# Kernel optimization log

Measured on AMD Instinct MI355X. Metric: run time of the kernel, lower is better.

Reference implementation:

```python
import jax, jax.numpy as jnp
import numpy as np

B, T = 32, 64            # batch, max_timesteps
D_EMB, D_CONTENT, D_STYLE = 512, 128, 16
VOCAB = 32000
TEMP = 1.0
SOS_IDX = 0


def setup_inputs() -> dict:
    key = jax.random.key(0)
    ks = jax.random.split(key, 8)
    s = 0.02  # small init scale to keep softmax well-conditioned
    d_in = D_EMB + D_CONTENT + D_STYLE
    return {
        "content": jax.random.normal(ks[0], (B, D_CONTENT), jnp.float32),
        "style": jax.random.normal(ks[1], (B, D_STYLE), jnp.float32),
        "E": jax.random.normal(ks[2], (VOCAB, D_EMB), jnp.float32) * s,
        "Wk": jax.random.normal(ks[3], (d_in, 4 * D_EMB), jnp.float32) * s,
        "Wr": jax.random.normal(ks[4], (D_EMB, 4 * D_EMB), jnp.float32) * s,
        "b": jnp.zeros((4 * D_EMB,), jnp.float32),
        "Ws": jax.random.normal(ks[5], (D_EMB, VOCAB), jnp.float32) * s,
        "bs": jnp.zeros((VOCAB,), jnp.float32),
    }


def reference(content, style, E, Wk, Wr, b, Ws, bs):
    sos_emb = jnp.broadcast_to(E[SOS_IDX], (B, D_EMB))  # start token embedding

    def step(carry, _):
        h, c, emb = carry
        x = jnp.concatenate([emb, content, style], axis=-1)   # [B, d_in]
        z = x @ Wk + h @ Wr + b                               # [B, 4*units]
        i, f, g, o = jnp.split(z, 4, axis=-1)                  # keras gate order i,f,c,o
        i = jax.nn.sigmoid(i)
        f = jax.nn.sigmoid(f)
        g = jnp.tanh(g)
        o = jax.nn.sigmoid(o)
        c = f * c + i * g
        h = o * jnp.tanh(c)
        logits = h @ Ws + bs                                   # [B, vocab]
        p = jax.nn.softmax(logits / TEMP, axis=-1)
        emb_next = p @ E                                       # soft embedding [B, d_emb]
        return (h, c, emb_next), emb_next

    h0 = jnp.zeros((B, D_EMB), content.dtype)
    c0 = jnp.zeros((B, D_EMB), content.dtype)
    _, embs = jax.lax.scan(step, (h0, c0, sos_emb), None, length=T - 1)
    # [T-1, B, D] -> [B, T-1, D]; prepend SOS embedding
    out = jnp.concatenate([sos_emb[:, None, :], jnp.transpose(embs, (1, 0, 2))], axis=1)
    return out  # [B, T, d_emb]
```

## Files before the change

kernel.cpp:

```cpp
#include <hip/hip_runtime.h>

#define T_STEPS 63
#define NWG 256
#define WG_SIZE 256
#define NA 32
#define NV 224
#define NJC 14
#define NDC 16

typedef float floatx4 __attribute__((ext_vector_type(4)));
typedef __bf16 bf16x8 __attribute__((ext_vector_type(8)));

__device__ __forceinline__ unsigned short f2bf(float x) {
  unsigned int u = __builtin_bit_cast(unsigned int, x);
  u += 0x7fffu + ((u >> 16) & 1u);
  return (unsigned short)(u >> 16);
}
__device__ __forceinline__ float sigmoidf(float x) {
  return 1.0f / (1.0f + __expf(-x));
}
__device__ __forceinline__ floatx4 mfma_bf16(bf16x8 a, bf16x8 b, floatx4 c) {
  return __builtin_amdgcn_mfma_f32_16x16x32_bf16(a, b, c, 0, 0, 0);
}
__device__ __forceinline__ floatx4 mfma_fp8(long a, long b, floatx4 c) {
  return __builtin_amdgcn_mfma_f32_16x16x32_fp8_fp8(a, b, c, 0, 0, 0);
}
__device__ __forceinline__ unsigned char f2fp8(float x) {
  return (unsigned char)(__builtin_amdgcn_cvt_pk_fp8_f32(x, x, 0, false) & 0xff);
}

__device__ __forceinline__ unsigned long long ald64(const void* p) {
  return __hip_atomic_load((const unsigned long long*)p, __ATOMIC_RELAXED, __HIP_MEMORY_SCOPE_AGENT);
}
__device__ __forceinline__ float aldf(const float* p) {
  return __hip_atomic_load(p, __ATOMIC_RELAXED, __HIP_MEMORY_SCOPE_AGENT);
}
__device__ __forceinline__ void astf(float* p, float v) {
  __hip_atomic_store(p, v, __ATOMIC_RELAXED, __HIP_MEMORY_SCOPE_AGENT);
}
__device__ __forceinline__ void astu16(unsigned short* p, unsigned short v) {
  __hip_atomic_store(p, v, __ATOMIC_RELAXED, __HIP_MEMORY_SCOPE_AGENT);
}
__device__ __forceinline__ void astu32(unsigned int* p, unsigned int v) {
  __hip_atomic_store(p, v, __ATOMIC_RELAXED, __HIP_MEMORY_SCOPE_AGENT);
}
__device__ __forceinline__ void astu8(unsigned char* p, unsigned char v) {
  __hip_atomic_store(p, v, __ATOMIC_RELAXED, __HIP_MEMORY_SCOPE_AGENT);
}
__device__ __forceinline__ void afaddf(float* p, float v) {
  __hip_atomic_fetch_add(p, v, __ATOMIC_RELAXED, __HIP_MEMORY_SCOPE_AGENT);
}
__device__ __forceinline__ bf16x8 ld_bf8_at(const void* p) {
  union { unsigned long long q[2]; bf16x8 v; } u;
  u.q[0] = ald64(p);
  u.q[1] = ald64((const char*)p + 8);
  return u.v;
}

__device__ __forceinline__ void signal_flag(int* f) {
  __builtin_amdgcn_s_waitcnt(0);
  __syncthreads();
  if (threadIdx.x == 0)
    __hip_atomic_fetch_add(f, 1, __ATOMIC_RELAXED, __HIP_MEMORY_SCOPE_AGENT);
}
__device__ __forceinline__ void wait_flag(const int* f, int target) {
  if (threadIdx.x == 0) {
    while (__hip_atomic_load(f, __ATOMIC_RELAXED, __HIP_MEMORY_SCOPE_AGENT) < target)
      __builtin_amdgcn_s_sleep(2);
  }
  __syncthreads();
}

__global__ void k_transpose(const float* __restrict__ in, unsigned short* __restrict__ out,
                            int R, int C, int ostride, int ooff) {
  __shared__ unsigned short tile[64][65];
  const int r0 = blockIdx.x << 6, c0 = blockIdx.y << 6;
  const int t = threadIdx.x;
  const int tr4 = t >> 6, tc = t & 63;
#pragma unroll
  for (int p = 0; p < 16; ++p) {
    int i = (p << 2) + tr4;
    int r = r0 + i;
    unsigned short v = 0;
    if (r < R) v = f2bf(in[(size_t)r * C + (c0 + tc)]);
    tile[i][tc] = v;
  }
  __syncthreads();
#pragma unroll
  for (int p = 0; p < 16; ++p) {
    int j = (p << 2) + tr4;
    int r = r0 + tc;
    if (r < R) out[(size_t)(c0 + j) * ostride + ooff + r] = tile[tc][j];
  }
}

__global__ void k_transpose_fp8(const float* __restrict__ in, unsigned char* __restrict__ out,
                                int R, int C, long OS) {
  __shared__ unsigned char tile[64][68];
  const int r0 = blockIdx.x << 6, c0 = blockIdx.y << 6;
  const int t = threadIdx.x;
  const int tr4 = t >> 6, tc = t & 63;
#pragma unroll
  for (int p = 0; p < 16; ++p) {
    int i = (p << 2) + tr4;
    int r = r0 + i;
    float v = (r < R) ? in[(size_t)r * C + (c0 + tc)] : 0.f;
    tile[i][tc] = f2fp8(v);
  }
  __syncthreads();
#pragma unroll
  for (int p = 0; p < 16; ++p) {
    int j = (p << 2) + tr4;
    out[(size_t)(c0 + j) * OS + r0 + tc] = tile[tc][j];
  }
}

__global__ void k_init(const float* __restrict__ content, const float* __restrict__ style,
                       const float* __restrict__ E, unsigned short* cs_bf, float* out) {
  const int stride = gridDim.x * blockDim.x;
  const int idx = blockIdx.x * blockDim.x + threadIdx.x;
  for (int i = idx; i < 32 * 160; i += stride) {
    int b = i / 160, k = i - b * 160;
    float v = 0.f;
    if (k < 128)      v = content[b * 128 + k];
    else if (k < 144) v = style[b * 16 + (k - 128)];
    cs_bf[i] = f2bf(v);
  }
  for (int i = idx; i < 32 * 512; i += stride) {
    int b = i >> 9, d = i & 511;
    out[(size_t)b * (64 * 512) + d] = E[d];
  }
}

#define SMEM_BYTES 160768
#define OFF_E8TS_L 73728
#define OFF_ELDS_L 147456
#define OFF_ZBUF_L 152576

__global__ void __launch_bounds__(WG_SIZE, 1) k_main(
    const float* __restrict__ bvec,
    const float* __restrict__ bs,
    const unsigned char* __restrict__ Ws8_g,
    const unsigned char* __restrict__ E8T_g,
    const unsigned short* __restrict__ WkrT,
    const unsigned short* __restrict__ cs_bf,
    const float* __restrict__ E,
    unsigned short* h_bufg,
    unsigned char* h8,
    unsigned short* emb_bf,
    unsigned char* e8g,
    float* Upart,
    float* Zbuf,
    int* hflag, int* eflag, int* qflag, int* pvflag,
    float* out)
{
  const int wg = blockIdx.x;
  const int t  = threadIdx.x;
  const int wv = t >> 6;
  const int lane = t & 63;
  const int q = lane >> 4;
  const int m16 = lane & 15;

  __shared__ __align__(16) char smem[SMEM_BYTES];
  unsigned char* lds_ws   = (unsigned char*)smem;
  unsigned char* lds_e8ts = (unsigned char*)(smem + OFF_E8TS_L);
  unsigned char* lds_e    = (unsigned char*)(smem + OFF_ELDS_L);
  unsigned short* lds_wkr = (unsigned short*)smem;
  float* zbuf = (float*)(smem + OFF_ZBUF_L);

  if (wg < NA) {
    for (int idx = t; idx < 64 * 148; idx += WG_SIZE) {
      int row = idx / 148, grp = idx - row * 148;
      int g = row >> 4, c = row & 15;
      int n = g * 512 + (wg << 4) + c;
      ulong2 v = *(const ulong2*)(WkrT + (size_t)n * 1184 + grp * 8);
      *(ulong2*)((char*)lds_wkr + row * 2384 + grp * 16) = v;
    }
    const int dl = t & 15;
    const float bias0 = bvec[0 * 512 + (wg << 4) + dl];
    const float bias1 = bvec[1 * 512 + (wg << 4) + dl];
    const float bias2 = bvec[2 * 512 + (wg << 4) + dl];
    const float bias3 = bvec[3 * 512 + (wg << 4) + dl];
    float c2[2] = {0.f, 0.f};
    __syncthreads();

    const int mt = wv & 1, g0 = (wv >> 1) << 1;
    const int row = mt * 16 + m16;
    const unsigned short* b0row = lds_wkr + (g0 * 16 + m16) * 1192;
    const unsigned short* b1row = lds_wkr + ((g0 + 1) * 16 + m16) * 1192;
    const int d = (wg << 4) + dl;
    const int dc_a = wg >> 1;
    const int dl32 = ((wg & 1) << 4) + dl;

    for (int s = 0; s < T_STEPS; ++s) {
      const int pc = s & 1;
      if (s > 0) {
        wait_flag(eflag + (s - 1) * 16, NA);
        if (t < NJC) astf(Zbuf + ((s - 1) & 1) * (NJC * 32) + t * 32 + wg, 0.0f);
      }
      floatx4 accG0 = {0.f, 0.f, 0.f, 0.f}, accG1 = {0.f, 0.f, 0.f, 0.f};
      if (s == 0) {
#pragma unroll 4
        for (int ks = 0; ks < 16; ++ks) {
          const float* ep = E + ks * 32 + q * 8;
          bf16x8 a;
#pragma unroll
          for (int i = 0; i < 8; ++i) a[i] = (__bf16)ep[i];
          accG0 = mfma_bf16(a, *(const bf16x8*)(b0row + ks * 32 + q * 8), accG0);
          accG1 = mfma_bf16(a, *(const bf16x8*)(b1row + ks * 32 + q * 8), accG1);
        }
      } else {
#pragma unroll 4
        for (int ks = 0; ks < 16; ++ks) {
          bf16x8 a = ld_bf8_at(emb_bf + row * 512 + ks * 32 + q * 8);
          accG0 = mfma_bf16(a, *(const bf16x8*)(b0row + ks * 32 + q * 8), accG0);
          accG1 = mfma_bf16(a, *(const bf16x8*)(b1row + ks * 32 + q * 8), accG1);
        }
      }
#pragma unroll
      for (int ks = 16; ks < 21; ++ks) {
        bf16x8 a = *(const bf16x8*)(cs_bf + row * 160 + (ks - 16) * 32 + q * 8);
        accG0 = mfma_bf16(a, *(const bf16x8*)(b0row + ks * 32 + q * 8), accG0);
        accG1 = mfma_bf16(a, *(const bf16x8*)(b1row + ks * 32 + q * 8), accG1);
      }
      if (s > 0) {
#pragma unroll 4
        for (int ks = 21; ks < 37; ++ks) {
          bf16x8 a = ld_bf8_at(h_bufg + row * 512 + (ks - 21) * 32 + q * 8);
          accG0 = mfma_bf16(a, *(const bf16x8*)(b0row + ks * 32 + q * 8), accG0);
          accG1 = mfma_bf16(a, *(const bf16x8*)(b1row + ks * 32 + q * 8), accG1);
        }
      }
#pragma unroll
      for (int r = 0; r < 4; ++r) {
        zbuf[(g0 * 32 + mt * 16 + q * 4 + r) * 16 + m16] = accG0[r];
        zbuf[((g0 + 1) * 32 + mt * 16 + q * 4 + r) * 16 + m16] = accG1[r];
      }
      __syncthreads();
#pragma unroll
      for (int pp = 0; pp < 2; ++pp) {
        const int b = (pp * 256 + t) >> 4;
        float zi = zbuf[(0 * 32 + b) * 16 + dl] + bias0;
        float zf = zbuf[(1 * 32 + b) * 16 + dl] + bias1;
        float zg = zbuf[(2 * 32 + b) * 16 + dl] + bias2;
        float zo = zbuf[(3 * 32 + b) * 16 + dl] + bias3;
        float iv = sigmoidf(zi), fv = sigmoidf(zf);
        float gv = tanhf(zg),    ov = sigmoidf(zo);
        c2[pp] = fv * c2[pp] + iv * gv;
        float h = ov * tanhf(c2[pp]);
        astu16(h_bufg + b * 512 + d, f2bf(h));
        astu8(h8 + b * 512 + d, f2fp8(h));
      }
      signal_flag(hflag + s * 16);
      wait_flag(pvflag + (s * NDC + dc_a) * 16, NJC);
#pragma unroll
      for (int pp = 0; pp < 2; ++pp) {
        const int b = (pp * 256 + t) >> 4;
        float uv = 0.f, Zv = 0.f;
        const float* up = Upart + ((size_t)(dc_a * NJC) * 32 + b) * 32 + dl32;
#pragma unroll
        for (int g = 0; g < NJC; ++g) uv += aldf(up + g * 1024);
#pragma unroll
        for (int g = 0; g < NJC; ++g) Zv += aldf(Zbuf + pc * (NJC * 32) + g * 32 + b);
        float ev = uv / Zv;
        out[(size_t)b * (64 * 512) + (size_t)(s + 1) * 512 + d] = ev;
        astu16(emb_bf + b * 512 + d, f2bf(ev));
      }
      signal_flag(eflag + s * 16);
    }
  } else {
    const int wgv = wg - NA;
    const int jc = wgv >> 4;
    const int dc = wgv & 15;
    const long j0 = (long)wgv * 144;
    for (int idx = t; idx < 144 * 64; idx += WG_SIZE) {
      int row = idx >> 6, grp = idx & 63;
      long v = *(const long*)(Ws8_g + (j0 + row) * 512 + grp * 8);
      *(long*)(lds_ws + row * 512 + ((grp ^ (row & 7)) << 3)) = v;
    }
    for (int idx = t; idx < 32 * 288; idx += WG_SIZE) {
      int dd = idx / 288, g = idx - dd * 288;
      long v = *(const long*)(E8T_g + (size_t)(dc * 32 + dd) * 32768 + (size_t)jc * 2304 + (size_t)g * 8);
      int g2 = g + dd; if (g2 >= 288) g2 -= 288;
      *(long*)(lds_e8ts + dd * 2304 + (g2 << 3)) = v;
    }
    for (int idx = t; idx < (32 * 160) / 8; idx += WG_SIZE) ((long*)lds_e)[idx] = 0;
    __syncthreads();

    for (int s = 0; s < T_STEPS; ++s) {
      wait_flag(hflag + s * 16, NA);
      const int pc = s & 1;
      long ah[2][16];
#pragma unroll
      for (int mtl = 0; mtl < 2; ++mtl)
#pragma unroll
        for (int ks = 0; ks < 16; ++ks)
          ah[mtl][ks] = (long)ald64(h8 + (mtl * 16 + m16) * 512 + ks * 32 + q * 8);
      for (int tile = wv; tile < 9; tile += 4) {
        const int jl = tile * 16 + m16;
        const unsigned char* wrow = lds_ws + jl * 512;
        const int sw = jl & 7;
        floatx4 acc[2] = {{0,0,0,0},{0,0,0,0}};
#pragma unroll
        for (int ks = 0; ks < 16; ++ks) {
          int g = ks * 4 + q;
          long bfrag = *(const long*)(wrow + ((g ^ sw) << 3));
          acc[0] = mfma_fp8(ah[0][ks], bfrag, acc[0]);
          acc[1] = mfma_fp8(ah[1][ks], bfrag, acc[1]);
        }
        const long jg = j0 + jl;
        const float bsv = bs[jg < 32000 ? jg : 31999];
        const bool valid = (jg < 32000);
#pragma unroll
        for (int mtl = 0; mtl < 2; ++mtl)
#pragma unroll
          for (int r = 0; r < 4; ++r) {
            float e = valid ? __expf(acc[mtl][r] + bsv) : 0.0f;
            lds_e[(mtl * 16 + q * 4 + r) * 160 + jl] = f2fp8(e);
          }
      }
      __syncthreads();
      for (int idx = t; idx < 32 * 36; idx += WG_SIZE) {
        int b = idx / 36, g = idx - b * 36;
        unsigned int v = *(const unsigned int*)(lds_e + b * 160 + g * 4);
        astu32((unsigned int*)(e8g + (size_t)b * 32768 + j0 + g * 4), v);
      }
      if (t >= 192 && t < 224) {
        const int b = t - 192;
        const unsigned int* rowp = (const unsigned int*)(lds_e + b * 160);
        float z = 0.f;
        for (int g = 0; g < 36; ++g) {
          int w4 = (int)rowp[g];
          z += __builtin_amdgcn_cvt_f32_fp8(w4, 0) + __builtin_amdgcn_cvt_f32_fp8(w4, 1)
             + __builtin_amdgcn_cvt_f32_fp8(w4, 2) + __builtin_amdgcn_cvt_f32_fp8(w4, 3);
        }
        afaddf(Zbuf + pc * (NJC * 32) + jc * 32 + b, z);
      }
      signal_flag(qflag + (s * NJC + jc) * 16);
      wait_flag(qflag + (s * NJC + jc) * 16, 16);
      {
        const int mtp = wv & 1, ntl = wv >> 1;
        const int dl_local = ntl * 16 + m16;
        const unsigned char* erow = lds_e8ts + dl_local * 2304;
        const unsigned char* arow = e8g + (size_t)(mtp * 16 + m16) * 32768 + (size_t)jc * 2304;
        floatx4 acc0 = {0,0,0,0}, acc1 = {0,0,0,0};
#pragma unroll 8
        for (int ks = 0; ks < 72; ks += 2) {
          long a0 = (long)ald64(arow + ks * 32 + q * 8);
          long a1 = (long)ald64(arow + (ks + 1) * 32 + q * 8);
          int g0 = ks * 4 + q + dl_local; if (g0 >= 288) g0 -= 288;
          int g1 = g0 + 4;                if (g1 >= 288) g1 -= 288;
          acc0 = mfma_fp8(a0, *(const long*)(erow + (g0 << 3)), acc0);
          acc1 = mfma_fp8(a1, *(const long*)(erow + (g1 << 3)), acc1);
        }
        floatx4 accs = acc0 + acc1;
#pragma unroll
        for (int r = 0; r < 4; ++r)
          astf(Upart + ((size_t)(dc * NJC + jc) * 32 + (mtp * 16 + q * 4 + r)) * 32 + dl_local, accs[r]);
      }
      signal_flag(pvflag + (s * NDC + dc) * 16);
    }
  }
}

extern "C" void kernel_launch(void* const* d_in, const int* in_sizes, int n_in,
                              void* d_out, int out_size, void* d_ws, size_t ws_size,
                              hipStream_t stream) {
  const float* content = (const float*)d_in[0];
  const float* style   = (const float*)d_in[1];
  const float* E       = (const float*)d_in[2];
  const float* Wk      = (const float*)d_in[3];
  const float* Wr      = (const float*)d_in[4];
  const float* bvec    = (const float*)d_in[5];
  const float* Ws      = (const float*)d_in[6];
  const float* bs      = (const float*)d_in[7];
  float* out = (float*)d_out;
  char* ws = (char*)d_ws;

  constexpr size_t SZ_WS8  = 32256ull * 512;
  constexpr size_t SZ_E8T  = 512ull * 32768;
  constexpr size_t SZ_WKRT = 2048ull * 1184 * 2;
  constexpr size_t SZ_CS   = 32ull * 160 * 2;
  constexpr size_t SZ_HB   = 32ull * 512 * 2;
  constexpr size_t SZ_H8   = 32ull * 512;
  constexpr size_t SZ_E8G  = 32ull * 32768;
  constexpr size_t SZ_UP   = 16ull * 14 * 32 * 32 * 4;
  constexpr size_t SZ_ZB   = 2ull * 14 * 32 * 4;
  constexpr size_t SZ_HF   = 64ull * 16 * 4;
  constexpr size_t SZ_EF   = 64ull * 16 * 4;
  constexpr size_t SZ_QF   = 63ull * 14 * 16 * 4;
  constexpr size_t SZ_PF   = 63ull * 16 * 16 * 4;
  constexpr size_t SZ_EMB  = 32ull * 512 * 2;
  constexpr size_t OFF_WS8  = 0;
  constexpr size_t OFF_E8T  = OFF_WS8 + SZ_WS8;
  constexpr size_t OFF_WKRT = OFF_E8T + SZ_E8T;
  constexpr size_t OFF_CS   = OFF_WKRT + SZ_WKRT;
  constexpr size_t OFF_HB   = OFF_CS + SZ_CS;
  constexpr size_t OFF_H8   = OFF_HB + SZ_HB;
  constexpr size_t OFF_E8G  = OFF_H8 + SZ_H8;
  constexpr size_t OFF_UP   = OFF_E8G + SZ_E8G;
  constexpr size_t OFF_ZB   = OFF_UP + SZ_UP;
  constexpr size_t OFF_HF   = OFF_ZB + SZ_ZB;
  constexpr size_t OFF_EF   = OFF_HF + SZ_HF;
  constexpr size_t OFF_QF   = OFF_EF + SZ_EF;
  constexpr size_t OFF_PF   = OFF_QF + SZ_QF;
  constexpr size_t OFF_EMB  = OFF_PF + SZ_PF;

  unsigned char*  Ws8_g = (unsigned char*)(ws + OFF_WS8);
  unsigned char*  E8T_g = (unsigned char*)(ws + OFF_E8T);
  unsigned short* WkrT  = (unsigned short*)(ws + OFF_WKRT);
  unsigned short* cs_bf = (unsigned short*)(ws + OFF_CS);
  unsigned short* h_bufg= (unsigned short*)(ws + OFF_HB);
  unsigned char*  h8    = (unsigned char*)(ws + OFF_H8);
  unsigned char*  e8g   = (unsigned char*)(ws + OFF_E8G);
  float* Upart          = (float*)(ws + OFF_UP);
  float* Zbuf           = (float*)(ws + OFF_ZB);
  int* hflag            = (int*)(ws + OFF_HF);
  int* eflag            = (int*)(ws + OFF_EF);
  int* qflag            = (int*)(ws + OFF_QF);
  int* pvflag           = (int*)(ws + OFF_PF);
  unsigned short* emb_bf= (unsigned short*)(ws + OFF_EMB);

  hipMemsetAsync(Ws8_g, 0, SZ_WS8, stream);
  hipMemsetAsync(E8T_g, 0, SZ_E8T, stream);
  hipMemsetAsync(WkrT, 0, SZ_WKRT, stream);
  hipMemsetAsync(ws + OFF_ZB, 0, SZ_ZB + SZ_HF + SZ_EF + SZ_QF + SZ_PF, stream);

  k_transpose_fp8<<<dim3(8, 500), 256, 0, stream>>>(Ws, Ws8_g, 512, 32000, 512);
  k_transpose_fp8<<<dim3(500, 8), 256, 0, stream>>>(E, E8T_g, 32000, 512, 32768);
  k_transpose<<<dim3(11, 32), 256, 0, stream>>>(Wk, WkrT, 656, 2048, 1184, 0);
  k_transpose<<<dim3(8, 32), 256, 0, stream>>>(Wr, WkrT, 512, 2048, 1184, 672);
  k_init<<<64, 256, 0, stream>>>(content, style, E, cs_bf, out);

  void* args[] = { (void*)&bvec, (void*)&bs, (void*)&Ws8_g, (void*)&E8T_g, (void*)&WkrT,
                   (void*)&cs_bf, (void*)&E, (void*)&h_bufg, (void*)&h8, (void*)&emb_bf,
                   (void*)&e8g, (void*)&Upart, (void*)&Zbuf,
                   (void*)&hflag, (void*)&eflag, (void*)&qflag, (void*)&pvflag,
                   (void*)&out };
  hipLaunchCooperativeKernel((void*)k_main, dim3(NWG), dim3(WG_SIZE), args, 0, stream);

  (void)in_sizes; (void)n_in; (void)out_size; (void)ws_size;
}
```

Baseline: 2.309 ms.

## Overlap recurrent h@Wr gate matmul with vocab phase and split h flags

Moves the recurrent h·Wr and content/style contributions of the next step's gate pre-activations so they are computed right after h is published, while the vocab workgroups compute softmax. Only the embedding part remains on the critical path after the e-flag wait. The single h flag is replaced by per-jc flag copies (NHM=15) to spread polling contention, and the output store is deferred until after signalling. This adds an extra wait on one h flag copy and more flag memory.

```diff
diff --git a/kernel.cpp b/kernel.cpp
--- a/kernel.cpp
+++ b/kernel.cpp
@@ -7,6 +7,7 @@
 #define NV 224
 #define NJC 14
 #define NDC 16
+#define NHM 15
 
 typedef float floatx4 __attribute__((ext_vector_type(4)));
 typedef __bf16 bf16x8 __attribute__((ext_vector_type(8)));
@@ -48,6 +49,9 @@
   __hip_atomic_store(p, v, __ATOMIC_RELAXED, __HIP_MEMORY_SCOPE_AGENT);
 }
 __device__ __forceinline__ void afaddf(float* p, float v) {
+  __hip_atomic_fetch_add(p, v, __ATOMIC_RELAXED, __HIP_MEMORY_SCOPE_AGENT);
+}
+__device__ __forceinline__ void afaddi(int* p, int v) {
   __hip_atomic_fetch_add(p, v, __ATOMIC_RELAXED, __HIP_MEMORY_SCOPE_AGENT);
 }
 __device__ __forceinline__ bf16x8 ld_bf8_at(const void* p) {
@@ -192,14 +196,17 @@
     const int dc_a = wg >> 1;
     const int dl32 = ((wg & 1) << 4) + dl;
 
+    floatx4 accG0 = {0.f, 0.f, 0.f, 0.f}, accG1 = {0.f, 0.f, 0.f, 0.f};
+
     for (int s = 0; s < T_STEPS; ++s) {
       const int pc = s & 1;
-      if (s > 0) {
-        wait_flag(eflag + (s - 1) * 16, NA);
-        if (t < NJC) astf(Zbuf + ((s - 1) & 1) * (NJC * 32) + t * 32 + wg, 0.0f);
-      }
-      floatx4 accG0 = {0.f, 0.f, 0.f, 0.f}, accG1 = {0.f, 0.f, 0.f, 0.f};
       if (s == 0) {
+#pragma unroll
+        for (int ks = 16; ks < 21; ++ks) {
+          bf16x8 a = *(const bf16x8*)(cs_bf + row * 160 + (ks - 16) * 32 + q * 8);
+          accG0 = mfma_bf16(a, *(const bf16x8*)(b0row + ks * 32 + q * 8), accG0);
+          accG1 = mfma_bf16(a, *(const bf16x8*)(b1row + ks * 32 + q * 8), accG1);
+        }
 #pragma unroll 4
         for (int ks = 0; ks < 16; ++ks) {
           const float* ep = E + ks * 32 + q * 8;
@@ -210,23 +217,11 @@
           accG1 = mfma_bf16(a, *(const bf16x8*)(b1row + ks * 32 + q * 8), accG1);
         }
       } else {
-#pragma unroll 4
+        wait_flag(eflag + (s - 1) * 16, NA);
+        if (t < NJC) astf(Zbuf + ((s - 1) & 1) * (NJC * 32) + t * 32 + wg, 0.0f);
+#pragma unroll 8
         for (int ks = 0; ks < 16; ++ks) {
           bf16x8 a = ld_bf8_at(emb_bf + row * 512 + ks * 32 + q * 8);
-          accG0 = mfma_bf16(a, *(const bf16x8*)(b0row + ks * 32 + q * 8), accG0);
-          accG1 = mfma_bf16(a, *(const bf16x8*)(b1row + ks * 32 + q * 8), accG1);
-        }
-      }
-#pragma unroll
-      for (int ks = 16; ks < 21; ++ks) {
-        bf16x8 a = *(const bf16x8*)(cs_bf + row * 160 + (ks - 16) * 32 + q * 8);
-        accG0 = mfma_bf16(a, *(const bf16x8*)(b0row + ks * 32 + q * 8), accG0);
-        accG1 = mfma_bf16(a, *(const bf16x8*)(b1row + ks * 32 + q * 8), accG1);
-      }
-      if (s > 0) {
-#pragma unroll 4
-        for (int ks = 21; ks < 37; ++ks) {
-          bf16x8 a = ld_bf8_at(h_bufg + row * 512 + (ks - 21) * 32 + q * 8);
           accG0 = mfma_bf16(a, *(const bf16x8*)(b0row + ks * 32 + q * 8), accG0);
           accG1 = mfma_bf16(a, *(const bf16x8*)(b1row + ks * 32 + q * 8), accG1);
         }
@@ -251,8 +246,28 @@
         astu16(h_bufg + b * 512 + d, f2bf(h));
         astu8(h8 + b * 512 + d, f2fp8(h));
       }
-      signal_flag(hflag + s * 16);
+      __builtin_amdgcn_s_waitcnt(0);
+      __syncthreads();
+      if (t < NHM) afaddi(hflag + (s * NHM + t) * 16, 1);
+      if (s + 1 < T_STEPS) {
+        wait_flag(hflag + (s * NHM + (NHM - 1)) * 16, NA);
+        accG0 = floatx4{0.f, 0.f, 0.f, 0.f};
+        accG1 = floatx4{0.f, 0.f, 0.f, 0.f};
+#pragma unroll 8
+        for (int ks = 21; ks < 37; ++ks) {
+          bf16x8 a = ld_bf8_at(h_bufg + row * 512 + (ks - 21) * 32 + q * 8);
+          accG0 = mfma_bf16(a, *(const bf16x8*)(b0row + ks * 32 + q * 8), accG0);
+          accG1 = mfma_bf16(a, *(const bf16x8*)(b1row + ks * 32 + q * 8), accG1);
+        }
+#pragma unroll
+        for (int ks = 16; ks < 21; ++ks) {
+          bf16x8 a = *(const bf16x8*)(cs_bf + row * 160 + (ks - 16) * 32 + q * 8);
+          accG0 = mfma_bf16(a, *(const bf16x8*)(b0row + ks * 32 + q * 8), accG0);
+          accG1 = mfma_bf16(a, *(const bf16x8*)(b1row + ks * 32 + q * 8), accG1);
+        }
+      }
       wait_flag(pvflag + (s * NDC + dc_a) * 16, NJC);
+      float evs[2];
 #pragma unroll
       for (int pp = 0; pp < 2; ++pp) {
         const int b = (pp * 256 + t) >> 4;
@@ -263,10 +278,15 @@
 #pragma unroll
         for (int g = 0; g < NJC; ++g) Zv += aldf(Zbuf + pc * (NJC * 32) + g * 32 + b);
         float ev = uv / Zv;
-        out[(size_t)b * (64 * 512) + (size_t)(s + 1) * 512 + d] = ev;
+        evs[pp] = ev;
         astu16(emb_bf + b * 512 + d, f2bf(ev));
       }
       signal_flag(eflag + s * 16);
+#pragma unroll
+      for (int pp = 0; pp < 2; ++pp) {
+        const int b = (pp * 256 + t) >> 4;
+        out[(size_t)b * (64 * 512) + (size_t)(s + 1) * 512 + d] = evs[pp];
+      }
     }
   } else {
     const int wgv = wg - NA;
@@ -288,7 +308,7 @@
     __syncthreads();
 
     for (int s = 0; s < T_STEPS; ++s) {
-      wait_flag(hflag + s * 16, NA);
+      wait_flag(hflag + (s * NHM + jc) * 16, NA);
       const int pc = s & 1;
       long ah[2][16];
 #pragma unroll
@@ -386,7 +406,7 @@
   constexpr size_t SZ_E8G  = 32ull * 32768;
   constexpr size_t SZ_UP   = 16ull * 14 * 32 * 32 * 4;
   constexpr size_t SZ_ZB   = 2ull * 14 * 32 * 4;
-  constexpr size_t SZ_HF   = 64ull * 16 * 4;
+  constexpr size_t SZ_HF   = 64ull * 15 * 16 * 4;
   constexpr size_t SZ_EF   = 64ull * 16 * 4;
   constexpr size_t SZ_QF   = 63ull * 14 * 16 * 4;
   constexpr size_t SZ_PF   = 63ull * 16 * 16 * 4;
```

After: 2.072 ms. 1.11x faster.
